# Kernel tuning notes

Measured on AMD Instinct MI355X. Metric: run time of the kernel, lower is better.

The kernel has to match this reference:

```python
import jax, jax.numpy as jnp
import numpy as np

NUMOBJECTS, EMB, H, E, T = 1000, 128, 128, 8, 2
N = 4096

def _ln(x, g, b, eps=1e-5):
    mu = jnp.mean(x, axis=-1, keepdims=True)
    var = jnp.var(x, axis=-1, keepdims=True)
    return (x - mu) * jax.lax.rsqrt(var + eps) * g + b

def setup_inputs() -> dict:
    key = jax.random.key(0)
    ks = jax.random.split(key, 16)
    s = lambda fan_in: 1.0 / np.sqrt(fan_in)
    return {
        "adjacency_matrix": jax.random.uniform(ks[0], (E, N, N), jnp.float32),
        "node_states": jax.random.normal(ks[1], (N, 2 * EMB), jnp.float32),
        "node_ids": jax.random.randint(ks[2], (N,), 0, NUMOBJECTS),
        "emb_table": jax.random.normal(ks[3], (NUMOBJECTS, EMB), jnp.float32) * 0.02,
        "W_init": jax.random.normal(ks[4], (3 * EMB, H), jnp.float32) * s(3 * EMB),
        "b_init": jnp.zeros((H,), jnp.float32),
        "W_out": jax.random.normal(ks[5], (E, H, H), jnp.float32) * s(H),
        "b_out": jnp.zeros((E, H), jnp.float32),
        "W_in": jax.random.normal(ks[6], (E, H, H), jnp.float32) * s(H),
        "b_in": jnp.zeros((E, H), jnp.float32),
        "Wx": jax.random.normal(ks[7], (2 * E * H, 3 * H), jnp.float32) * s(2 * E * H),
        "bx": jnp.zeros((3 * H,), jnp.float32),
        "Wh": jax.random.normal(ks[8], (H, 3 * H), jnp.float32) * s(H),
        "bh": jnp.zeros((3 * H,), jnp.float32),
        "ln_gamma": jnp.ones((3, H), jnp.float32),
        "ln_beta": jnp.zeros((3, H), jnp.float32),
    }

def _gru(x, h, Wx, bx, Wh, bh, g, b):
    gi = x @ Wx + bx                      # [N, 3H]
    gh = h @ Wh + bh                      # [N, 3H]
    ir, iz, inn = jnp.split(gi, 3, axis=-1)
    hr, hz, hn = jnp.split(gh, 3, axis=-1)
    r = jax.nn.sigmoid(_ln(ir + hr, g[0], b[0]))
    z = jax.nn.sigmoid(_ln(iz + hz, g[1], b[1]))
    n = jnp.tanh(_ln(inn + r * hn, g[2], b[2]))
    return (1.0 - z) * n + z * h

def reference(adjacency_matrix, node_states, node_ids, emb_table, W_init, b_init,
              W_out, b_out, W_in, b_in, Wx, bx, Wh, bh, ln_gamma, ln_beta):
    emb = emb_table[node_ids]                                   # [N, EMB]
    node_init = jnp.concatenate([emb, node_states], axis=1)     # [N, 3*EMB]
    h = jnp.tanh(node_init @ W_init + b_init)                   # [N, H]
    A_out = adjacency_matrix                                    # [E, N, N]
    A_in = jnp.transpose(adjacency_matrix, (0, 2, 1))
    n_nodes = h.shape[0]
    for _ in range(T):
        # grouped per-edge-type FC + Tanh, then adjacency message passing
        ho = jnp.tanh(jnp.einsum('nh,ehk->enk', h, W_out) + b_out[:, None, :])
        mo = jnp.einsum('enm,emk->nek', A_out, ho).reshape(n_nodes, -1)  # [N, E*H]
        hi = jnp.tanh(jnp.einsum('nh,ehk->enk', h, W_in) + b_in[:, None, :])
        mi = jnp.einsum('enm,emk->nek', A_in, hi).reshape(n_nodes, -1)
        msg = jnp.concatenate([mo, mi], axis=1)                 # [N, 2*E*H]
        h = _gru(msg, h, Wx, bx, Wh, bh, ln_gamma, ln_beta)
    return h
```

## Files before the change

### kernel.cpp

```cpp
#include <hip/hip_runtime.h>
#include <stdint.h>

#define NNODES 4096
#define HDIM   128
#define NE     8
#define KXX    2176
#define NG     512
#define NKT    34

typedef unsigned short u16;
typedef _Float16 f16;
typedef f16   h8v __attribute__((ext_vector_type(8)));
typedef float f4v __attribute__((ext_vector_type(4)));

static __device__ __forceinline__ u16 hbits(f16 h) {
    union { f16 h; u16 u; } x; x.h = h; return x.u;
}
static __device__ __forceinline__ f16 h_of(u16 u) {
    union { u16 u; f16 h; } x; x.u = u; return x.h;
}
static __device__ __forceinline__ int swz(int r, int c) {
    return r * 64 + (c ^ ((((r >> 3) ^ r) & 7) << 3));
}
static __device__ __forceinline__ f4v mfma16h(h8v a, h8v b, f4v c) {
    return __builtin_amdgcn_mfma_f32_16x16x32_f16(a, b, c, 0, 0, 0);
}
static __device__ __forceinline__ h8v lds_frag(const u16* p) {
    return *(const h8v*)p;
}
static __device__ __forceinline__ void ncvt8h(const float* g, u16* vh) {
    float4 v0 = *(const float4*)g, v1 = *(const float4*)(g + 4);
    float vs[8] = {v0.x, v0.y, v0.z, v0.w, v1.x, v1.y, v1.z, v1.w};
    #pragma unroll
    for (int q = 0; q < 8; q++) vh[q] = hbits((f16)vs[q]);
}
static __device__ __forceinline__ void stage_tile16(const u16* __restrict__ g, u16* l, int tid) {
    const int lane = tid & 63, wv = tid >> 6;
    #pragma unroll
    for (int q = 0; q < 4; q++) {
        __builtin_amdgcn_global_load_lds(
            (__attribute__((address_space(1))) void*)(g + ((size_t)((wv * 4 + q) * 64 + lane)) * 8),
            (__attribute__((address_space(3))) void*)(l + (wv * 4 + q) * 512),
            16, 0, 0);
    }
}
static __device__ __forceinline__ void stage_tile8(const u16* __restrict__ g, u16* l, int tid) {
    const int lane = tid & 63, wv = tid >> 6;
    #pragma unroll
    for (int q = 0; q < 2; q++) {
        __builtin_amdgcn_global_load_lds(
            (__attribute__((address_space(1))) void*)(g + ((size_t)((wv * 2 + q) * 64 + lane)) * 8),
            (__attribute__((address_space(3))) void*)(l + (wv * 2 + q) * 512),
            16, 0, 0);
    }
}

__global__ void k0_init(const float* __restrict__ nst, const int* __restrict__ ids,
                        const float* __restrict__ emb, const float* __restrict__ Wi,
                        const float* __restrict__ bi, float* __restrict__ h,
                        u16* __restrict__ Xh)
{
    __shared__ float ni[16][384];
    const int n0 = blockIdx.x * 16;
    const int tid = threadIdx.x;
    for (int idx = tid; idx < 16 * 384; idx += 128) {
        int r = idx / 384, c = idx - r * 384;
        float v;
        if (c < 128) v = emb[(size_t)ids[n0 + r] * 128 + c];
        else         v = nst[(size_t)(n0 + r) * 256 + (c - 128)];
        ni[r][c] = v;
    }
    __syncthreads();
    float acc[16];
    #pragma unroll
    for (int r = 0; r < 16; r++) acc[r] = 0.f;
    for (int c = 0; c < 384; c++) {
        float w = Wi[c * 128 + tid];
        #pragma unroll
        for (int r = 0; r < 16; r++) acc[r] += ni[r][c] * w;
    }
    float bb = bi[tid];
    const int kt = 32 + (tid >> 6), cl = tid & 63;
    #pragma unroll
    for (int r = 0; r < 16; r++) {
        const int n = n0 + r;
        float v = tanhf(acc[r] + bb);
        h[(size_t)n * HDIM + tid] = v;
        Xh[(size_t)(n >> 6) * NKT * 4096 + kt * 4096 + swz(n & 63, cl)] = hbits((f16)v);
    }
}

__global__ void kprep(const float* __restrict__ Wx, const float* __restrict__ bx,
                      const float* __restrict__ Wh, const float* __restrict__ bh,
                      u16* __restrict__ WTt, float* __restrict__ bv)
{
    const int j = blockIdx.x;
    const int ct = j >> 7, jl = j & 127;
    for (int c = threadIdx.x; c < KXX; c += blockDim.x) {
        float v;
        if (j < 384) {
            if (c < 2048) v = Wx[(size_t)c * 384 + j];
            else          v = (j < 256) ? Wh[(size_t)(c - 2048) * 384 + j] : 0.f;
        } else {
            if (c < 2048) v = 0.f;
            else          v = Wh[(size_t)(c - 2048) * 384 + (j - 128)];
        }
        WTt[(size_t)(ct * NKT + (c >> 6)) * 8192 + swz(jl, c & 63)] = hbits((f16)v);
    }
    if (threadIdx.x == 0) {
        float b;
        if (j < 256)      b = bx[j] + bh[j];
        else if (j < 384) b = bx[j];
        else              b = bh[j - 128];
        bv[j] = b;
    }
}

__global__ void kprepW(const float* __restrict__ Wo, const float* __restrict__ Wn,
                       u16* __restrict__ Wp)
{
    const int de = blockIdx.x;
    const int dir = de >> 3, e = de & 7;
    const float* W = (dir ? Wn : Wo) + (size_t)e * HDIM * HDIM;
    u16* dst = Wp + (size_t)de * 2 * 8192;
    for (int idx = threadIdx.x; idx < HDIM * HDIM; idx += blockDim.x) {
        int j = idx >> 7, k = idx & 127;
        dst[(size_t)(j >> 6) * 8192 + swz(k, j & 63)] = hbits((f16)W[idx]);
    }
}

__global__ void kpa(const float* __restrict__ A, u16* __restrict__ AT0,
                    u16* __restrict__ AT1)
{
    const int b = blockIdx.x;
    const int mb = b & 63, nt = (b >> 6) & 31, e = b >> 11;
    __shared__ u16 lf[64 * 136];
    const int tid = threadIdx.x;
    {
        const int rr = tid >> 2, cb = (tid & 3) * 32;
        const float* src = A + (size_t)e * NNODES * NNODES
                             + (size_t)(mb * 64 + rr) * NNODES + nt * 128 + cb;
        u16 hv[32];
        #pragma unroll
        for (int q = 0; q < 8; q++) {
            float4 v = *(const float4*)(src + q * 4);
            hv[q * 4 + 0] = hbits((f16)v.x); hv[q * 4 + 1] = hbits((f16)v.y);
            hv[q * 4 + 2] = hbits((f16)v.z); hv[q * 4 + 3] = hbits((f16)v.w);
        }
        const int arow = mb * 64 + rr;
        const int mc0 = nt * 2 + (cb >> 6), cl0 = cb & 63;
        const size_t tb0 = (((size_t)e * 32 + (arow >> 7)) * 64 + mc0) * 8192;
        const int rl = arow & 127;
        #pragma unroll
        for (int g = 0; g < 4; g++)
            *(uint4*)&AT0[tb0 + swz(rl, cl0 + 8 * g)] = *(const uint4*)&hv[8 * g];
        #pragma unroll
        for (int g = 0; g < 4; g++)
            *(uint4*)&lf[rr * 136 + cb + 8 * g] = *(const uint4*)&hv[8 * g];
    }
    __syncthreads();
    {
        const size_t tb1 = (((size_t)e * 32 + nt) * 64 + mb) * 8192;
        const int r = tid >> 3, c = (tid & 7) * 8;
        #pragma unroll
        for (int p = 0; p < 4; p++) {
            const int nl = r + 32 * p;
            u16 vv[8];
            #pragma unroll
            for (int q = 0; q < 8; q++) vv[q] = lf[(c + q) * 136 + nl];
            *(uint4*)&AT1[tb1 + swz(nl, c)] = *(const uint4*)vv;
        }
    }
}

__global__ __launch_bounds__(256, 3) void k1_hoT(const float* __restrict__ h,
        const u16* __restrict__ Wp, const float* __restrict__ bo,
        const float* __restrict__ bn, u16* __restrict__ hoT)
{
    const int mt = blockIdx.x, e = blockIdx.y, dir = blockIdx.z;
    const float* bias = (dir == 0 ? bo : bn) + (size_t)e * HDIM;
    const u16* Wt = Wp + (size_t)(dir * NE + e) * 2 * 8192;
    const int m0 = mt * 128;
    const int tid = threadIdx.x, lane = tid & 63, wv = tid >> 6;
    const int wrow0 = (wv & 1) * 64, wcol0 = (wv >> 1) * 64;
    const int lrow = lane & 15, lkb = (lane >> 4) * 8;

    __shared__ __align__(16) u16 lWT[128 * 64];
    __shared__ __align__(16) u16 lB [128 * 64];

    f4v acc[4][4];
    #pragma unroll
    for (int i = 0; i < 4; i++)
        #pragma unroll
        for (int j = 0; j < 4; j++)
            #pragma unroll
            for (int q = 0; q < 4; q++) acc[i][j][q] = 0.f;

    for (int jt = 0; jt < 128; jt += 64) {
        __syncthreads();
        stage_tile16(Wt + (size_t)(jt >> 6) * 8192, lWT, tid);
        {
            int m = tid >> 3;
            int jc = (tid & 7) * 8;
            #pragma unroll
            for (int p = 0; p < 4; p++) {
                u16 vh[8];
                ncvt8h(h + (size_t)(m0 + m + 32 * p) * HDIM + jt + jc, vh);
                *(uint4*)&lB[swz(m + 32 * p, jc)] = *(const uint4*)vh;
            }
        }
        __syncthreads();
        #pragma unroll
        for (int ks = 0; ks < 2; ks++) {
            const int kb = ks * 32 + lkb;
            h8v a[4], b8[4];
            #pragma unroll
            for (int i = 0; i < 4; i++)
                a[i] = lds_frag(&lWT[swz(wrow0 + 16 * i + lrow, kb)]);
            #pragma unroll
            for (int j = 0; j < 4; j++)
                b8[j] = lds_frag(&lB[swz(wcol0 + 16 * j + lrow, kb)]);
            #pragma unroll
            for (int i = 0; i < 4; i++)
                #pragma unroll
                for (int j = 0; j < 4; j++)
                    acc[i][j] = mfma16h(a[i], b8[j], acc[i][j]);
        }
    }
    u16* dst = hoT + (size_t)(dir * NE + e) * 64 * 8192;
    #pragma unroll
    for (int i = 0; i < 4; i++)
        #pragma unroll
        for (int j = 0; j < 4; j++)
            #pragma unroll
            for (int reg = 0; reg < 4; reg++) {
                int k = wrow0 + 16 * i + (lane >> 4) * 4 + reg;
                int m = m0 + wcol0 + 16 * j + (lane & 15);
                float v = tanhf(acc[i][j][reg] + bias[k]);
                dst[(size_t)(m >> 6) * 8192 + swz(k, m & 63)] = hbits((f16)v);
            }
}

__global__ __launch_bounds__(256, 4) void k2n(const float* __restrict__ A,
        const u16* __restrict__ AT0, const u16* __restrict__ AT1,
        const u16* __restrict__ hoT, u16* __restrict__ Xh, int pre)
{
    const int l = blockIdx.x;
    const int x = l & 7, i = l >> 3;
    const int c = x * 2 + (i >> 6), nt64 = i & 63;
    const int e = c & 7, dir = c >> 3;
    const int n0 = nt64 * 64;
    const int tid = threadIdx.x, lane = tid & 63, wv = tid >> 6;
    const int wrow0 = (wv & 1) * 32, wcol0 = (wv >> 1) * 64;
    const int lrow = lane & 15, lkb = (lane >> 4) * 8;

    __shared__ __align__(16) u16 lA[64 * 64];
    __shared__ __align__(16) u16 lB[128 * 64];

    const float* Ae = A + (size_t)e * NNODES * NNODES;
    const u16* Bt0 = hoT + (size_t)(dir * NE + e) * 64 * 8192;
    const u16* Tp  = (dir ? AT1 : AT0)
                   + (((size_t)e * 32 + (nt64 >> 1)) * 64) * 8192 + (nt64 & 1) * 4096;

    f4v acc[2][4];
    #pragma unroll
    for (int ii = 0; ii < 2; ii++)
        #pragma unroll
        for (int j = 0; j < 4; j++)
            #pragma unroll
            for (int q = 0; q < 4; q++) acc[ii][j][q] = 0.f;

    for (int mc = 0; mc < 64; mc++) {
        const int m0 = mc * 64;
        __syncthreads();
        stage_tile16(Bt0 + (size_t)mc * 8192, lB, tid);
        if (pre) {
            stage_tile8(Tp + (size_t)mc * 8192, lA, tid);
        } else if (dir == 0) {
            const int r = tid >> 2, cc = (tid & 3) * 16;
            #pragma unroll
            for (int p = 0; p < 2; p++) {
                u16 vh[8];
                ncvt8h(Ae + (size_t)(n0 + r) * NNODES + m0 + cc + 8 * p, vh);
                *(uint4*)&lA[swz(r, cc + 8 * p)] = *(const uint4*)vh;
            }
        } else {
            const int mm = tid >> 2, nn = (tid & 3) * 16;
            #pragma unroll
            for (int p = 0; p < 2; p++) {
                u16 vh[8];
                ncvt8h(Ae + (size_t)(m0 + mm) * NNODES + n0 + nn + 8 * p, vh);
                #pragma unroll
                for (int q = 0; q < 8; q++)
                    lA[swz(nn + 8 * p + q, mm)] = vh[q];
            }
        }
        __syncthreads();
        #pragma unroll
        for (int ks = 0; ks < 2; ks++) {
            const int kb = ks * 32 + lkb;
            h8v ah[2], b8[4];
            #pragma unroll
            for (int ii = 0; ii < 2; ii++)
                ah[ii] = lds_frag(&lA[swz(wrow0 + 16 * ii + lrow, kb)]);
            #pragma unroll
            for (int j = 0; j < 4; j++)
                b8[j] = lds_frag(&lB[swz(wcol0 + 16 * j + lrow, kb)]);
            #pragma unroll
            for (int ii = 0; ii < 2; ii++)
                #pragma unroll
                for (int j = 0; j < 4; j++)
                    acc[ii][j] = mfma16h(ah[ii], b8[j], acc[ii][j]);
        }
    }
    u16* xt = Xh + (size_t)nt64 * NKT * 4096;
    #pragma unroll
    for (int ii = 0; ii < 2; ii++)
        #pragma unroll
        for (int j = 0; j < 4; j++)
            #pragma unroll
            for (int reg = 0; reg < 4; reg++) {
                int row = wrow0 + 16 * ii + (lane >> 4) * 4 + reg;
                int C = dir * 1024 + e * 128 + wcol0 + 16 * j + (lane & 15);
                xt[(size_t)(C >> 6) * 4096 + swz(row, C & 63)] =
                    hbits((f16)acc[ii][j][reg]);
            }
}

__global__ __launch_bounds__(256, 4) void k3_gates(const u16* __restrict__ Xh,
        const u16* __restrict__ WTt, float* __restrict__ G0,
        float* __restrict__ G1)
{
    const int nt = blockIdx.x, ct = blockIdx.y, kk = blockIdx.z;
    const int n0 = nt * 64, j0 = ct * 128;
    const int kt0 = kk ? 17 : 0, kt1 = kk ? NKT : 17;
    float* G = kk ? G1 : G0;
    const int tid = threadIdx.x, lane = tid & 63, wv = tid >> 6;
    const int wrow0 = (wv & 1) * 32, wcol0 = (wv >> 1) * 64;
    const int lrow = lane & 15, lkb = (lane >> 4) * 8;
    __shared__ __align__(16) u16 lX[64 * 64];
    __shared__ __align__(16) u16 lW[128 * 64];

    f4v acc[2][4];
    #pragma unroll
    for (int i = 0; i < 2; i++)
        #pragma unroll
        for (int j = 0; j < 4; j++)
            #pragma unroll
            for (int q = 0; q < 4; q++) acc[i][j][q] = 0.f;

    for (int kt = kt0; kt < kt1; kt++) {
        __syncthreads();
        stage_tile8(Xh + ((size_t)nt * NKT + kt) * 4096, lX, tid);
        stage_tile16(WTt + (size_t)(ct * NKT + kt) * 8192, lW, tid);
        __syncthreads();
        #pragma unroll
        for (int ks = 0; ks < 2; ks++) {
            const int kb = ks * 32 + lkb;
            h8v ah[2], b8[4];
            #pragma unroll
            for (int i = 0; i < 2; i++)
                ah[i] = lds_frag(&lX[swz(wrow0 + 16 * i + lrow, kb)]);
            #pragma unroll
            for (int j = 0; j < 4; j++)
                b8[j] = lds_frag(&lW[swz(wcol0 + 16 * j + lrow, kb)]);
            #pragma unroll
            for (int i = 0; i < 2; i++)
                #pragma unroll
                for (int j = 0; j < 4; j++)
                    acc[i][j] = mfma16h(ah[i], b8[j], acc[i][j]);
        }
    }
    #pragma unroll
    for (int i = 0; i < 2; i++)
        #pragma unroll
        for (int j = 0; j < 4; j++)
            #pragma unroll
            for (int reg = 0; reg < 4; reg++) {
                int row = wrow0 + 16 * i + (lane >> 4) * 4 + reg;
                int col = wcol0 + 16 * j + (lane & 15);
                G[(size_t)(n0 + row) * NG + j0 + col] = acc[i][j][reg];
            }
}

__global__ void k4_ln(const float* __restrict__ G0, const float* __restrict__ G1,
                      const float* __restrict__ bv, const float* __restrict__ gam,
                      const float* __restrict__ bet, float* __restrict__ h,
                      u16* __restrict__ Xh, float* __restrict__ out)
{
    const int n = blockIdx.x * 4 + (threadIdx.x >> 6);
    const int t = threadIdx.x & 63;
    const float* g0 = G0 + (size_t)n * NG;
    const float* g1 = G1 + (size_t)n * NG;
    auto gv = [&](int c) { return g0[c] + g1[c] + bv[c]; };
    float a0 = gv(t),       a0b = gv(t + 64);
    float a1 = gv(128 + t), a1b = gv(192 + t);
    float a2 = gv(256 + t), a2b = gv(320 + t);
    float a3 = gv(384 + t), a3b = gv(448 + t);

    auto redsum = [](float v) {
        #pragma unroll
        for (int m = 32; m >= 1; m >>= 1) v += __shfl_xor(v, m, 64);
        return v;
    };

    float s0 = redsum(a0 + a0b) * (1.f / 128.f);
    float q0 = redsum(a0 * a0 + a0b * a0b) * (1.f / 128.f);
    float rs0 = rsqrtf(fmaxf(q0 - s0 * s0, 0.f) + 1e-5f);
    float x0  = (a0  - s0) * rs0 * gam[t]      + bet[t];
    float x0b = (a0b - s0) * rs0 * gam[t + 64] + bet[t + 64];
    float r  = 1.f / (1.f + expf(-x0));
    float rb = 1.f / (1.f + expf(-x0b));

    float s1 = redsum(a1 + a1b) * (1.f / 128.f);
    float q1 = redsum(a1 * a1 + a1b * a1b) * (1.f / 128.f);
    float rs1 = rsqrtf(fmaxf(q1 - s1 * s1, 0.f) + 1e-5f);
    float x1  = (a1  - s1) * rs1 * gam[128 + t] + bet[128 + t];
    float x1b = (a1b - s1) * rs1 * gam[192 + t] + bet[192 + t];
    float z  = 1.f / (1.f + expf(-x1));
    float zb = 1.f / (1.f + expf(-x1b));

    float c2  = a2  + r  * a3;
    float c2b = a2b + rb * a3b;
    float s2 = redsum(c2 + c2b) * (1.f / 128.f);
    float q2 = redsum(c2 * c2 + c2b * c2b) * (1.f / 128.f);
    float rs2 = rsqrtf(fmaxf(q2 - s2 * s2, 0.f) + 1e-5f);
    float x2  = (c2  - s2) * rs2 * gam[256 + t] + bet[256 + t];
    float x2b = (c2b - s2) * rs2 * gam[320 + t] + bet[320 + t];
    float nn  = tanhf(x2);
    float nnb = tanhf(x2b);

    float ho  = h[(size_t)n * HDIM + t];
    float hob = h[(size_t)n * HDIM + t + 64];
    float hn  = (1.f - z)  * nn  + z  * ho;
    float hnb = (1.f - zb) * nnb + zb * hob;
    h[(size_t)n * HDIM + t]      = hn;
    h[(size_t)n * HDIM + t + 64] = hnb;
    u16* xt = Xh + (size_t)(n >> 6) * NKT * 4096;
    xt[32 * 4096 + swz(n & 63, t)] = hbits((f16)hn);
    xt[33 * 4096 + swz(n & 63, t)] = hbits((f16)hnb);
    out[(size_t)n * HDIM + t]      = hn;
    out[(size_t)n * HDIM + t + 64] = hnb;
}

extern "C" void kernel_launch(void* const* d_in, const int* in_sizes, int n_in,
                              void* d_out, int out_size, void* d_ws, size_t ws_size,
                              hipStream_t stream)
{
    const float* A    = (const float*)d_in[0];
    const float* nst  = (const float*)d_in[1];
    const int*   ids  = (const int*)d_in[2];
    const float* emb  = (const float*)d_in[3];
    const float* Wi   = (const float*)d_in[4];
    const float* bi   = (const float*)d_in[5];
    const float* Wo   = (const float*)d_in[6];
    const float* bo   = (const float*)d_in[7];
    const float* Wn   = (const float*)d_in[8];
    const float* bn   = (const float*)d_in[9];
    const float* Wx   = (const float*)d_in[10];
    const float* bx   = (const float*)d_in[11];
    const float* Wh   = (const float*)d_in[12];
    const float* bh   = (const float*)d_in[13];
    const float* gam  = (const float*)d_in[14];
    const float* bet  = (const float*)d_in[15];

    char* ws = (char*)d_ws;
    size_t off = 0;
    auto alloc = [&](size_t bytes) {
        size_t cur = off; off += (bytes + 255) & ~(size_t)255; return (void*)(ws + cur);
    };
    float* h   = (float*)alloc((size_t)NNODES * HDIM * 4);
    u16*   hoT = (u16*)  alloc((size_t)2 * NE * 64 * 8192 * 2);
    u16*   Xh  = (u16*)  alloc((size_t)64 * NKT * 4096 * 2);
    float* G0  = (float*)alloc((size_t)NNODES * NG * 4);
    float* G1  = (float*)alloc((size_t)NNODES * NG * 4);
    u16*   WTt = (u16*)  alloc((size_t)4 * NKT * 8192 * 2);
    float* bv  = (float*)alloc((size_t)NG * 4);
    u16*   Wp  = (u16*)  alloc((size_t)16 * 2 * 8192 * 2);
    size_t need0 = off;
    u16*   AT0 = (u16*)  alloc((size_t)NE * NNODES * NNODES * 2);
    u16*   AT1 = (u16*)  alloc((size_t)NE * NNODES * NNODES * 2);
    size_t need1 = off;

    int pre;
    if      (ws_size >= need1) pre = 1;
    else if (ws_size >= need0) pre = 0;
    else return;

    kprep<<<512, 256, 0, stream>>>(Wx, bx, Wh, bh, WTt, bv);
    kprepW<<<16, 256, 0, stream>>>(Wo, Wn, Wp);
    k0_init<<<256, 128, 0, stream>>>(nst, ids, emb, Wi, bi, h, Xh);
    if (pre) kpa<<<16384, 256, 0, stream>>>(A, AT0, AT1);
    for (int it = 0; it < 2; it++) {
        k1_hoT<<<dim3(32, 8, 2), 256, 0, stream>>>(h, Wp, bo, bn, hoT);
        k2n<<<1024, 256, 0, stream>>>(A, AT0, AT1, hoT, Xh, pre);
        k3_gates<<<dim3(64, 4, 2), 256, 0, stream>>>(Xh, WTt, G0, G1);
        k4_ln<<<1024, 256, 0, stream>>>(G0, G1, bv, gam, bet, h, Xh, (float*)d_out);
    }
    (void)in_sizes; (void)n_in; (void)out_size;
}
```

Before: 1.294 ms.

## Double-buffer LDS tiles in GEMM kernels to overlap staging with MFMA

The message-passing and gate GEMM kernels (k2n, k3_gates) now use two LDS buffers. The next k-tile is staged while MFMAs run on the current one, which removes one __syncthreads per iteration. k1_hoT now stages both K halves up front and syncs once. LDS per block doubles, so launch-bound occupancy targets are lowered. The single sync per iteration relies on the staging loads landing before the next barrier, which holds because staging is a synchronous load-then-store into LDS.

Measured after the change: 1.339 ms. 1.03x slower.

```diff
diff --git a/kernel.cpp b/kernel.cpp
--- a/kernel.cpp
+++ b/kernel.cpp
@@ -15,9 +15,6 @@
 
 static __device__ __forceinline__ u16 hbits(f16 h) {
     union { f16 h; u16 u; } x; x.h = h; return x.u;
-}
-static __device__ __forceinline__ f16 h_of(u16 u) {
-    union { u16 u; f16 h; } x; x.u = u; return x.h;
 }
 static __device__ __forceinline__ int swz(int r, int c) {
     return r * 64 + (c ^ ((((r >> 3) ^ r) & 7) << 3));
@@ -173,7 +170,7 @@
     }
 }
 
-__global__ __launch_bounds__(256, 3) void k1_hoT(const float* __restrict__ h,
+__global__ __launch_bounds__(256, 2) void k1_hoT(const float* __restrict__ h,
         const u16* __restrict__ Wp, const float* __restrict__ bo,
         const float* __restrict__ bn, u16* __restrict__ hoT)
 {
@@ -185,8 +182,8 @@
     const int wrow0 = (wv & 1) * 64, wcol0 = (wv >> 1) * 64;
     const int lrow = lane & 15, lkb = (lane >> 4) * 8;
 
-    __shared__ __align__(16) u16 lWT[128 * 64];
-    __shared__ __align__(16) u16 lB [128 * 64];
+    __shared__ __align__(16) u16 lWT[2][128 * 64];
+    __shared__ __align__(16) u16 lB [2][128 * 64];
 
     f4v acc[4][4];
     #pragma unroll
@@ -196,30 +193,32 @@
             #pragma unroll
             for (int q = 0; q < 4; q++) acc[i][j][q] = 0.f;
 
-    for (int jt = 0; jt < 128; jt += 64) {
-        __syncthreads();
-        stage_tile16(Wt + (size_t)(jt >> 6) * 8192, lWT, tid);
-        {
-            int m = tid >> 3;
-            int jc = (tid & 7) * 8;
-            #pragma unroll
-            for (int p = 0; p < 4; p++) {
-                u16 vh[8];
-                ncvt8h(h + (size_t)(m0 + m + 32 * p) * HDIM + jt + jc, vh);
-                *(uint4*)&lB[swz(m + 32 * p, jc)] = *(const uint4*)vh;
-            }
-        }
-        __syncthreads();
+    stage_tile16(Wt,        lWT[0], tid);
+    stage_tile16(Wt + 8192, lWT[1], tid);
+    #pragma unroll
+    for (int half = 0; half < 2; half++) {
+        int m = tid >> 3;
+        int jc = (tid & 7) * 8;
+        #pragma unroll
+        for (int p = 0; p < 4; p++) {
+            u16 vh[8];
+            ncvt8h(h + (size_t)(m0 + m + 32 * p) * HDIM + half * 64 + jc, vh);
+            *(uint4*)&lB[half][swz(m + 32 * p, jc)] = *(const uint4*)vh;
+        }
+    }
+    __syncthreads();
+    #pragma unroll
+    for (int half = 0; half < 2; half++) {
         #pragma unroll
         for (int ks = 0; ks < 2; ks++) {
             const int kb = ks * 32 + lkb;
             h8v a[4], b8[4];
             #pragma unroll
             for (int i = 0; i < 4; i++)
-                a[i] = lds_frag(&lWT[swz(wrow0 + 16 * i + lrow, kb)]);
+                a[i] = lds_frag(&lWT[half][swz(wrow0 + 16 * i + lrow, kb)]);
             #pragma unroll
             for (int j = 0; j < 4; j++)
-                b8[j] = lds_frag(&lB[swz(wcol0 + 16 * j + lrow, kb)]);
+                b8[j] = lds_frag(&lB[half][swz(wcol0 + 16 * j + lrow, kb)]);
             #pragma unroll
             for (int i = 0; i < 4; i++)
                 #pragma unroll
@@ -241,7 +240,7 @@
             }
 }
 
-__global__ __launch_bounds__(256, 4) void k2n(const float* __restrict__ A,
+__global__ __launch_bounds__(256, 3) void k2n(const float* __restrict__ A,
         const u16* __restrict__ AT0, const u16* __restrict__ AT1,
         const u16* __restrict__ hoT, u16* __restrict__ Xh, int pre)
 {
@@ -254,8 +253,8 @@
     const int wrow0 = (wv & 1) * 32, wcol0 = (wv >> 1) * 64;
     const int lrow = lane & 15, lkb = (lane >> 4) * 8;
 
-    __shared__ __align__(16) u16 lA[64 * 64];
-    __shared__ __align__(16) u16 lB[128 * 64];
+    __shared__ __align__(16) u16 lA[2][64 * 64];
+    __shared__ __align__(16) u16 lB[2][128 * 64];
 
     const float* Ae = A + (size_t)e * NNODES * NNODES;
     const u16* Bt0 = hoT + (size_t)(dir * NE + e) * 64 * 8192;
@@ -270,48 +269,53 @@
             #pragma unroll
             for (int q = 0; q < 4; q++) acc[ii][j][q] = 0.f;
 
-    for (int mc = 0; mc < 64; mc++) {
-        const int m0 = mc * 64;
-        __syncthreads();
-        stage_tile16(Bt0 + (size_t)mc * 8192, lB, tid);
+    auto STAGE = [&](int buf, int mc) {
+        stage_tile16(Bt0 + (size_t)mc * 8192, lB[buf], tid);
         if (pre) {
-            stage_tile8(Tp + (size_t)mc * 8192, lA, tid);
+            stage_tile8(Tp + (size_t)mc * 8192, lA[buf], tid);
         } else if (dir == 0) {
             const int r = tid >> 2, cc = (tid & 3) * 16;
             #pragma unroll
             for (int p = 0; p < 2; p++) {
                 u16 vh[8];
-                ncvt8h(Ae + (size_t)(n0 + r) * NNODES + m0 + cc + 8 * p, vh);
-                *(uint4*)&lA[swz(r, cc + 8 * p)] = *(const uint4*)vh;
+                ncvt8h(Ae + (size_t)(n0 + r) * NNODES + mc * 64 + cc + 8 * p, vh);
+                *(uint4*)&lA[buf][swz(r, cc + 8 * p)] = *(const uint4*)vh;
             }
         } else {
             const int mm = tid >> 2, nn = (tid & 3) * 16;
             #pragma unroll
             for (int p = 0; p < 2; p++) {
                 u16 vh[8];
-                ncvt8h(Ae + (size_t)(m0 + mm) * NNODES + n0 + nn + 8 * p, vh);
+                ncvt8h(Ae + (size_t)(mc * 64 + mm) * NNODES + n0 + nn + 8 * p, vh);
                 #pragma unroll
                 for (int q = 0; q < 8; q++)
-                    lA[swz(nn + 8 * p + q, mm)] = vh[q];
+                    lA[buf][swz(nn + 8 * p + q, mm)] = vh[q];
             }
         }
+    };
+
+    int cur = 0;
+    STAGE(0, 0);
+    for (int mc = 0; mc < 64; mc++) {
         __syncthreads();
+        if (mc + 1 < 64) STAGE(cur ^ 1, mc + 1);
         #pragma unroll
         for (int ks = 0; ks < 2; ks++) {
             const int kb = ks * 32 + lkb;
             h8v ah[2], b8[4];
             #pragma unroll
             for (int ii = 0; ii < 2; ii++)
-                ah[ii] = lds_frag(&lA[swz(wrow0 + 16 * ii + lrow, kb)]);
+                ah[ii] = lds_frag(&lA[cur][swz(wrow0 + 16 * ii + lrow, kb)]);
             #pragma unroll
             for (int j = 0; j < 4; j++)
-                b8[j] = lds_frag(&lB[swz(wcol0 + 16 * j + lrow, kb)]);
+                b8[j] = lds_frag(&lB[cur][swz(wcol0 + 16 * j + lrow, kb)]);
             #pragma unroll
             for (int ii = 0; ii < 2; ii++)
                 #pragma unroll
                 for (int j = 0; j < 4; j++)
                     acc[ii][j] = mfma16h(ah[ii], b8[j], acc[ii][j]);
         }
+        cur ^= 1;
     }
     u16* xt = Xh + (size_t)nt64 * NKT * 4096;
     #pragma unroll
@@ -327,7 +331,7 @@
             }
 }
 
-__global__ __launch_bounds__(256, 4) void k3_gates(const u16* __restrict__ Xh,
+__global__ __launch_bounds__(256, 3) void k3_gates(const u16* __restrict__ Xh,
         const u16* __restrict__ WTt, float* __restrict__ G0,
         float* __restrict__ G1)
 {
@@ -338,8 +342,8 @@
     const int tid = threadIdx.x, lane = tid & 63, wv = tid >> 6;
     const int wrow0 = (wv & 1) * 32, wcol0 = (wv >> 1) * 64;
     const int lrow = lane & 15, lkb = (lane >> 4) * 8;
-    __shared__ __align__(16) u16 lX[64 * 64];
-    __shared__ __align__(16) u16 lW[128 * 64];
+    __shared__ __align__(16) u16 lX[2][64 * 64];
+    __shared__ __align__(16) u16 lW[2][128 * 64];
 
     f4v acc[2][4];
     #pragma unroll
@@ -349,27 +353,33 @@
             #pragma unroll
             for (int q = 0; q < 4; q++) acc[i][j][q] = 0.f;
 
+    auto STAGE = [&](int buf, int kt) {
+        stage_tile8(Xh + ((size_t)nt * NKT + kt) * 4096, lX[buf], tid);
+        stage_tile16(WTt + (size_t)(ct * NKT + kt) * 8192, lW[buf], tid);
+    };
+
+    int cur = 0;
+    STAGE(0, kt0);
     for (int kt = kt0; kt < kt1; kt++) {
         __syncthreads();
-        stage_tile8(Xh + ((size_t)nt * NKT + kt) * 4096, lX, tid);
-        stage_tile16(WTt + (size_t)(ct * NKT + kt) * 8192, lW, tid);
-        __syncthreads();
+        if (kt + 1 < kt1) STAGE(cur ^ 1, kt + 1);
         #pragma unroll
         for (int ks = 0; ks < 2; ks++) {
             const int kb = ks * 32 + lkb;
             h8v ah[2], b8[4];
             #pragma unroll
             for (int i = 0; i < 2; i++)
-                ah[i] = lds_frag(&lX[swz(wrow0 + 16 * i + lrow, kb)]);
+                ah[i] = lds_frag(&lX[cur][swz(wrow0 + 16 * i + lrow, kb)]);
             #pragma unroll
             for (int j = 0; j < 4; j++)
-                b8[j] = lds_frag(&lW[swz(wcol0 + 16 * j + lrow, kb)]);
+                b8[j] = lds_frag(&lW[cur][swz(wcol0 + 16 * j + lrow, kb)]);
             #pragma unroll
             for (int i = 0; i < 2; i++)
                 #pragma unroll
                 for (int j = 0; j < 4; j++)
                     acc[i][j] = mfma16h(ah[i], b8[j], acc[i][j]);
         }
+        cur ^= 1;
     }
     #pragma unroll
     for (int i = 0; i < 2; i++)
```
